# Optimization experiments

Measured on AMD Instinct MI355X. Metric: run time of the kernel, lower is better.

The kernel has to match this reference:

```python
import jax, jax.numpy as jnp
import numpy as np

B, T, C, HS = 256, 256, 384, 64


def setup_inputs() -> dict:
    key = jax.random.key(0)
    k1, k2, k3, k4 = jax.random.split(key, 4)
    X = jax.random.normal(k1, (B, T, C), dtype=jnp.float32)
    Wq = jax.random.normal(k2, (C, HS), dtype=jnp.float32) * (C ** -0.5)
    Wk = jax.random.normal(k3, (C, HS), dtype=jnp.float32) * (C ** -0.5)
    Wv = jax.random.normal(k4, (C, HS), dtype=jnp.float32) * (C ** -0.5)
    return {"X": X, "Wq": Wq, "Wk": Wk, "Wv": Wv}


def reference(X, Wq, Wk, Wv):
    # Single causal self-attention head (dropout in eval mode / identity).
    num_channels = X.shape[-1]
    q = jnp.einsum('btc,ch->bth', X, Wq)  # [B,T,HS]
    k = jnp.einsum('btc,ch->bth', X, Wk)
    v = jnp.einsum('btc,ch->bth', X, Wv)
    # NOTE: original scales by embedding dim C**-0.5, not head_size**-0.5.
    scores = jnp.einsum('bqh,bkh->bqk', q, k) * (num_channels ** -0.5)  # [B,T,T]
    Tq = X.shape[1]
    causal = jnp.tril(jnp.ones((Tq, Tq), dtype=bool))
    scores = jnp.where(causal, scores, jnp.float32(-jnp.inf))
    weights = jax.nn.softmax(scores, axis=-1)
    return jnp.einsum('bqk,bkh->bqh', weights, v)  # [B,T,HS]
```

## Files before the change

### kernel.cpp

```cpp
#include <hip/hip_runtime.h>
#include <hip/hip_bf16.h>

#define B_  256
#define T_  256
#define C_  384
#define HS_ 64
#define BT_ (B_*T_)

typedef __attribute__((ext_vector_type(8))) short short8;
typedef __attribute__((ext_vector_type(4))) float f32x4;

__device__ __forceinline__ unsigned short f2bf(float f) {
    unsigned u = __float_as_uint(f);
    u += 0x7FFFu + ((u >> 16) & 1u);
    return (unsigned short)(u >> 16);
}

__global__ __launch_bounds__(256) void prep_wfrag(
    const float* __restrict__ Wq, const float* __restrict__ Wk,
    const float* __restrict__ Wv, unsigned short* __restrict__ Wfrag)
{
    const int tid  = blockIdx.x * 256 + threadIdx.x;
    const int lane = tid & 63;
    const int q    = tid >> 6;
    const int f    = q % 3;
    const int q2   = q / 3;
    const int wn   = q2 & 3;
    const int s    = q2 >> 2;

    const int n     = wn * 48 + f * 16 + (lane & 15);
    const int kbase = s * 32 + (lane >> 4) * 8;
    const float* src = (n < 64) ? Wq : (n < 128) ? Wk : Wv;
    const int c      = n & 63;
    const float scale = (n < 64) ? 0.05103103630798288f : 1.0f;

    short8 out;
    #pragma unroll
    for (int j = 0; j < 8; ++j)
        out[j] = (short)f2bf(src[(size_t)(kbase + j) * HS_ + c] * scale);
    *(short8*)&Wfrag[(size_t)tid * 8] = out;
}

#define LQ_OFF 0
#define LK_OFF 18432
#define LV_OFF 36864
#define LX_OFF 53760
#define LDSP   40

__global__ __launch_bounds__(1024, 4) void head_fused(
    const float* __restrict__ X, const unsigned short* __restrict__ Wfrag,
    float* __restrict__ out)
{
    __shared__ unsigned short lds[74240];
    const int t    = threadIdx.x;
    const int w    = t >> 6;
    const int lane = t & 63;
    const int lo   = lane & 15;
    const int hi   = lane >> 4;
    const int b    = blockIdx.x;
    const int wm   = w >> 2, wn = w & 3;

    const float* Xb = X + (size_t)b * T_ * C_;
    const short8* Wf = (const short8*)Wfrag;

    const int srow  = t >> 2;
    const int squad = t & 3;

    auto stage_load = [&](int k0, float4* g) {
        const float* p = Xb + (size_t)srow * C_ + k0 + squad * 8;
        g[0] = *(const float4*)(p);
        g[1] = *(const float4*)(p + 4);
    };
    auto stage_write = [&](int buf, const float4* g) {
        short8 p;
        p[0] = (short)f2bf(g[0].x); p[1] = (short)f2bf(g[0].y);
        p[2] = (short)f2bf(g[0].z); p[3] = (short)f2bf(g[0].w);
        p[4] = (short)f2bf(g[1].x); p[5] = (short)f2bf(g[1].y);
        p[6] = (short)f2bf(g[1].z); p[7] = (short)f2bf(g[1].w);
        *(short8*)&lds[LX_OFF + buf * 10240 + srow * 40 + squad * 8] = p;
    };
    auto load_w = [&](int s, short8* wf) {
        const short8* base = Wf + ((size_t)(s * 4 + wn) * 3) * 64 + lane;
        #pragma unroll
        for (int f = 0; f < 3; ++f)
            wf[f] = base[f * 64];
    };

    float4 g[2];
    short8 wf[3];
    stage_load(0, g);
    load_w(0, wf);
    stage_write(0, g);
    __syncthreads();

    f32x4 acc[4][3];
    #pragma unroll
    for (int m = 0; m < 4; ++m)
        #pragma unroll
        for (int f = 0; f < 3; ++f)
            acc[m][f] = (f32x4){0.f, 0.f, 0.f, 0.f};

    #pragma unroll 2
    for (int s = 0; s < 12; ++s) {
        const int cur = s & 1;
        float4 gn[2];
        short8 wfn[3];
        if (s < 11) {
            stage_load((s + 1) * 32, gn);
            load_w(s + 1, wfn);
        }
        short8 af[4];
        #pragma unroll
        for (int m = 0; m < 4; ++m)
            af[m] = *(const short8*)&lds[LX_OFF + cur * 10240 + (wm * 64 + m * 16 + lo) * 40 + hi * 8];
        #pragma unroll
        for (int m = 0; m < 4; ++m)
            #pragma unroll
            for (int f = 0; f < 3; ++f)
                acc[m][f] = __builtin_amdgcn_mfma_f32_16x16x32_bf16(af[m], wf[f], acc[m][f], 0, 0, 0);
        if (s < 11) {
            stage_write(cur ^ 1, gn);
            wf[0] = wfn[0]; wf[1] = wfn[1]; wf[2] = wfn[2];
        }
        __syncthreads();
    }

    #pragma unroll
    for (int m = 0; m < 4; ++m) {
        const int rowb = wm * 64 + m * 16 + hi * 4;
        #pragma unroll
        for (int f = 0; f < 3; ++f) {
            const int base = wn * 48 + f * 16;
            if (base < 64) {
                #pragma unroll
                for (int r = 0; r < 4; ++r)
                    lds[LQ_OFF + (rowb + r) * 72 + base + lo] = f2bf(acc[m][f][r]);
            } else if (base < 128) {
                #pragma unroll
                for (int r = 0; r < 4; ++r)
                    lds[LK_OFF + (rowb + r) * 72 + (base - 64) + lo] = f2bf(acc[m][f][r]);
            } else {
                ushort4 pk = { f2bf(acc[m][f][0]), f2bf(acc[m][f][1]),
                               f2bf(acc[m][f][2]), f2bf(acc[m][f][3]) };
                *(ushort4*)&lds[LV_OFF + (base - 128 + lo) * 264 + rowb] = pk;
            }
        }
    }
    __syncthreads();

    unsigned short* Pw = &lds[LX_OFF + w * 640];

    const int sg  = w & 3, pos = w >> 2;
    const int tq  = (pos == 0) ? sg : (pos == 1) ? 15 - sg : (pos == 2) ? 4 + sg : 11 - sg;

    {
        const int q_lane = tq * 16 + lo;
        short8 qf0 = *(const short8*)&lds[LQ_OFF + q_lane * 72 + hi * 8];
        short8 qf1 = *(const short8*)&lds[LQ_OFF + q_lane * 72 + hi * 8 + 32];

        f32x4 acc_o[4];
        #pragma unroll
        for (int n = 0; n < 4; ++n) acc_o[n] = (f32x4){0.f, 0.f, 0.f, 0.f};
        float Mr = -1e30f, Lr = 0.f;

        const int nsteps = (tq >> 1) + 1;
        for (int s = 0; s < nsteps; ++s) {
            const int kv0 = s * 32;
            f32x4 sb[2];
            sb[0] = (f32x4){0.f, 0.f, 0.f, 0.f};
            sb[1] = (f32x4){0.f, 0.f, 0.f, 0.f};
            #pragma unroll
            for (int n = 0; n < 2; ++n) {
                const unsigned short* kb = &lds[LK_OFF + (kv0 + n * 16 + lo) * 72 + hi * 8];
                short8 kf0 = *(const short8*)kb;
                short8 kf1 = *(const short8*)(kb + 32);
                sb[n] = __builtin_amdgcn_mfma_f32_16x16x32_bf16(kf0, qf0, sb[n], 0, 0, 0);
                sb[n] = __builtin_amdgcn_mfma_f32_16x16x32_bf16(kf1, qf1, sb[n], 0, 0, 0);
            }
            if (s == nsteps - 1) {
                #pragma unroll
                for (int n = 0; n < 2; ++n)
                    #pragma unroll
                    for (int r = 0; r < 4; ++r)
                        if (kv0 + n * 16 + hi * 4 + r > q_lane) sb[n][r] = -1e30f;
            }
            float pmax = fmaxf(fmaxf(fmaxf(sb[0][0], sb[0][1]), fmaxf(sb[0][2], sb[0][3])),
                               fmaxf(fmaxf(sb[1][0], sb[1][1]), fmaxf(sb[1][2], sb[1][3])));
            pmax = fmaxf(pmax, __shfl_xor(pmax, 16));
            pmax = fmaxf(pmax, __shfl_xor(pmax, 32));
            const float Mn = fmaxf(Mr, pmax);
            const float fr = __expf(Mr - Mn);
            Mr = Mn;
            float p0 = __expf(sb[0][0] - Mn), p1 = __expf(sb[0][1] - Mn);
            float p2 = __expf(sb[0][2] - Mn), p3 = __expf(sb[0][3] - Mn);
            float p4 = __expf(sb[1][0] - Mn), p5 = __expf(sb[1][1] - Mn);
            float p6 = __expf(sb[1][2] - Mn), p7 = __expf(sb[1][3] - Mn);
            float ls = ((p0 + p1) + (p2 + p3)) + ((p4 + p5) + (p6 + p7));
            ls += __shfl_xor(ls, 16);
            ls += __shfl_xor(ls, 32);
            Lr = Lr * fr + ls;
            #pragma unroll
            for (int n = 0; n < 4; ++n) {
                acc_o[n][0] *= fr; acc_o[n][1] *= fr;
                acc_o[n][2] *= fr; acc_o[n][3] *= fr;
            }
            ushort4 w0 = { f2bf(p0), f2bf(p1), f2bf(p2), f2bf(p3) };
            ushort4 w1 = { f2bf(p4), f2bf(p5), f2bf(p6), f2bf(p7) };
            *(ushort4*)&Pw[lo * LDSP + hi * 4]      = w0;
            *(ushort4*)&Pw[lo * LDSP + 16 + hi * 4] = w1;
            short8 pf = *(const short8*)&Pw[lo * LDSP + hi * 8];
            #pragma unroll
            for (int n = 0; n < 4; ++n) {
                short8 vf = *(const short8*)&lds[LV_OFF + (n * 16 + lo) * 264 + kv0 + hi * 8];
                acc_o[n] = __builtin_amdgcn_mfma_f32_16x16x32_bf16(vf, pf, acc_o[n], 0, 0, 0);
            }
        }
        const float inv = 1.0f / Lr;
        float* op = out + ((size_t)(b * 256 + q_lane)) * HS_;
        #pragma unroll
        for (int n = 0; n < 4; ++n)
            #pragma unroll
            for (int r = 0; r < 4; ++r)
                op[n * 16 + hi * 4 + r] = acc_o[n][r] * inv;
    }
}

extern "C" void kernel_launch(void* const* d_in, const int* in_sizes, int n_in,
                              void* d_out, int out_size, void* d_ws, size_t ws_size,
                              hipStream_t stream) {
    const float* X  = (const float*)d_in[0];
    const float* Wq = (const float*)d_in[1];
    const float* Wk = (const float*)d_in[2];
    const float* Wv = (const float*)d_in[3];
    float* out = (float*)d_out;

    unsigned short* Wfrag = (unsigned short*)d_ws;

    prep_wfrag<<<36, 256, 0, stream>>>(Wq, Wk, Wv, Wfrag);
    head_fused<<<B_, 1024, 0, stream>>>(X, Wfrag, out);
}
```

Baseline: 36.47 us.

## Deepen X prefetch, add lazy softmax rescale and MFMA priority hints

The projection loop now prefetches X two stages ahead in registers and writes the next LDS buffer before the MFMAs instead of after, so global latency is spread over more work. The attention loop skips the running-max update and accumulator rescale whenever every lane's new max stays within 8 of the old one, which removes multiplies and an exp in most steps. s_setprio is raised around the MFMA blocks so waves issuing matrix ops get priority. These changes add register pressure from the doubled prefetch buffers, and the lazy max lets exponent values grow up to e^8 before rescaling.

After: 36.04 us. About the same (-1.2%).

```diff
diff --git a/kernel.cpp b/kernel.cpp
--- a/kernel.cpp
+++ b/kernel.cpp
@@ -86,11 +86,12 @@
             wf[f] = base[f * 64];
     };
 
-    float4 g[2];
-    short8 wf[3];
-    stage_load(0, g);
-    load_w(0, wf);
-    stage_write(0, g);
+    float4 gx[2][2];
+    short8 wfr[2][3];
+    stage_load(0, gx[0]);
+    load_w(0, wfr[0]);
+    stage_load(32, gx[1]);
+    stage_write(0, gx[0]);
     __syncthreads();
 
     f32x4 acc[4][3];
@@ -103,12 +104,10 @@
     #pragma unroll 2
     for (int s = 0; s < 12; ++s) {
         const int cur = s & 1;
-        float4 gn[2];
-        short8 wfn[3];
-        if (s < 11) {
-            stage_load((s + 1) * 32, gn);
-            load_w(s + 1, wfn);
-        }
+        if (s < 10) stage_load((s + 2) * 32, gx[cur]);
+        if (s < 11) load_w(s + 1, wfr[cur ^ 1]);
+        if (s < 11) stage_write(cur ^ 1, gx[cur ^ 1]);
+
         short8 af[4];
         #pragma unroll
         for (int m = 0; m < 4; ++m)
@@ -117,11 +116,7 @@
         for (int m = 0; m < 4; ++m)
             #pragma unroll
             for (int f = 0; f < 3; ++f)
-                acc[m][f] = __builtin_amdgcn_mfma_f32_16x16x32_bf16(af[m], wf[f], acc[m][f], 0, 0, 0);
-        if (s < 11) {
-            stage_write(cur ^ 1, gn);
-            wf[0] = wfn[0]; wf[1] = wfn[1]; wf[2] = wfn[2];
-        }
+                acc[m][f] = __builtin_amdgcn_mfma_f32_16x16x32_bf16(af[m], wfr[cur][f], acc[m][f], 0, 0, 0);
         __syncthreads();
     }
 
@@ -169,6 +164,7 @@
             f32x4 sb[2];
             sb[0] = (f32x4){0.f, 0.f, 0.f, 0.f};
             sb[1] = (f32x4){0.f, 0.f, 0.f, 0.f};
+            __builtin_amdgcn_s_setprio(1);
             #pragma unroll
             for (int n = 0; n < 2; ++n) {
                 const unsigned short* kb = &lds[LK_OFF + (kv0 + n * 16 + lo) * 72 + hi * 8];
@@ -177,6 +173,7 @@
                 sb[n] = __builtin_amdgcn_mfma_f32_16x16x32_bf16(kf0, qf0, sb[n], 0, 0, 0);
                 sb[n] = __builtin_amdgcn_mfma_f32_16x16x32_bf16(kf1, qf1, sb[n], 0, 0, 0);
             }
+            __builtin_amdgcn_s_setprio(0);
             if (s == nsteps - 1) {
                 #pragma unroll
                 for (int n = 0; n < 2; ++n)
@@ -188,9 +185,20 @@
                                fmaxf(fmaxf(sb[1][0], sb[1][1]), fmaxf(sb[1][2], sb[1][3])));
             pmax = fmaxf(pmax, __shfl_xor(pmax, 16));
             pmax = fmaxf(pmax, __shfl_xor(pmax, 32));
-            const float Mn = fmaxf(Mr, pmax);
-            const float fr = __expf(Mr - Mn);
-            Mr = Mn;
+            float Mn;
+            if (__all(pmax - Mr <= 8.0f)) {
+                Mn = Mr;
+            } else {
+                Mn = fmaxf(Mr, pmax);
+                const float fr = __expf(Mr - Mn);
+                Mr = Mn;
+                Lr *= fr;
+                #pragma unroll
+                for (int n = 0; n < 4; ++n) {
+                    acc_o[n][0] *= fr; acc_o[n][1] *= fr;
+                    acc_o[n][2] *= fr; acc_o[n][3] *= fr;
+                }
+            }
             float p0 = __expf(sb[0][0] - Mn), p1 = __expf(sb[0][1] - Mn);
             float p2 = __expf(sb[0][2] - Mn), p3 = __expf(sb[0][3] - Mn);
             float p4 = __expf(sb[1][0] - Mn), p5 = __expf(sb[1][1] - Mn);
@@ -198,22 +206,19 @@
             float ls = ((p0 + p1) + (p2 + p3)) + ((p4 + p5) + (p6 + p7));
             ls += __shfl_xor(ls, 16);
             ls += __shfl_xor(ls, 32);
-            Lr = Lr * fr + ls;
-            #pragma unroll
-            for (int n = 0; n < 4; ++n) {
-                acc_o[n][0] *= fr; acc_o[n][1] *= fr;
-                acc_o[n][2] *= fr; acc_o[n][3] *= fr;
-            }
+            Lr += ls;
             ushort4 w0 = { f2bf(p0), f2bf(p1), f2bf(p2), f2bf(p3) };
             ushort4 w1 = { f2bf(p4), f2bf(p5), f2bf(p6), f2bf(p7) };
             *(ushort4*)&Pw[lo * LDSP + hi * 4]      = w0;
             *(ushort4*)&Pw[lo * LDSP + 16 + hi * 4] = w1;
             short8 pf = *(const short8*)&Pw[lo * LDSP + hi * 8];
+            __builtin_amdgcn_s_setprio(1);
             #pragma unroll
             for (int n = 0; n < 4; ++n) {
                 short8 vf = *(const short8*)&lds[LV_OFF + (n * 16 + lo) * 264 + kv0 + hi * 8];
                 acc_o[n] = __builtin_amdgcn_mfma_f32_16x16x32_bf16(vf, pf, acc_o[n], 0, 0, 0);
             }
+            __builtin_amdgcn_s_setprio(0);
         }
         const float inv = 1.0f / Lr;
         float* op = out + ((size_t)(b * 256 + q_lane)) * HS_;
```
